# Kernel tuning notes

Measured on AMD Instinct MI355X. Metric: run time of the kernel, lower is better.

Reference implementation:

```python
import jax, jax.numpy as jnp
import numpy as np

N = 100_000        # num nodes
E = 1_600_000      # num edges (self-loops appended in reference)
IN_DIM = 128
OUT_DIM = 128
NUM_HEAD = 8
D_HEAD = OUT_DIM // NUM_HEAD
NEG_SLOPE = 0.2
EPS = 1e-10


def setup_inputs() -> dict:
    key = jax.random.key(0)
    k1, k2, k3, k4, k5 = jax.random.split(key, 5)
    x = jax.random.normal(k1, (N, IN_DIM), dtype=jnp.float32)
    edge_list = jax.random.randint(k2, (E, 2), 0, N, dtype=jnp.int32)
    edge_weight = jax.random.uniform(k3, (E,), dtype=jnp.float32)
    # nn.Linear(input_dim, output_dim) params
    W = jax.random.normal(k4, (IN_DIM, OUT_DIM), dtype=jnp.float32) / np.sqrt(IN_DIM).astype(np.float32)
    b = jnp.zeros((OUT_DIM,), dtype=jnp.float32)
    # query: (num_head, 2*output_dim/num_head), kaiming-uniform-ish init
    query = jax.random.normal(k5, (NUM_HEAD, 2 * D_HEAD), dtype=jnp.float32) * 0.1
    return {"x": x, "edge_list": edge_list, "edge_weight": edge_weight,
            "W": W, "b": b, "query": query}


def reference(x, edge_list, edge_weight, W, b, query):
    # --- message ---
    self_idx = jnp.arange(N, dtype=edge_list.dtype)
    node_in = jnp.concatenate([edge_list[:, 0], self_idx])   # [E+N]
    node_out = jnp.concatenate([edge_list[:, 1], self_idx])  # [E+N]
    ew = jnp.concatenate([edge_weight, jnp.ones((N,), edge_weight.dtype)])[:, None]  # [E+N,1]

    hidden = x @ W + b                                        # [N, OUT_DIM]
    h_in = hidden[node_in]                                    # [E+N, OUT_DIM]
    h_out = hidden[node_out]                                  # [E+N, OUT_DIM]

    # torch: stack(..., dim=-1).view(-1, num_head, 2*d_head) -> interleaved layout
    key_ = jnp.stack([h_in, h_out], axis=-1).reshape(-1, NUM_HEAD, 2 * D_HEAD)
    w = jnp.einsum('hd,nhd->nh', query, key_)                 # [E+N, H]
    w = jax.nn.leaky_relu(w, NEG_SLOPE)

    seg_max = jax.ops.segment_max(w, node_out, num_segments=N)  # [N, H]
    w = w - seg_max[node_out]
    att = jnp.exp(w) * ew                                     # [E+N, H]

    counts = jax.ops.segment_sum(jnp.ones((node_out.shape[0],), att.dtype),
                                 node_out, num_segments=N)[:, None]  # [N,1] (>=1: self-loops)
    norm = jax.ops.segment_sum(att, node_out, num_segments=N) / counts  # scatter_mean
    att = att / (norm[node_out] + EPS)

    value = h_in.reshape(-1, NUM_HEAD, D_HEAD)
    message = (att[..., None] * value).reshape(-1, OUT_DIM)   # [E+N, OUT_DIM]

    # --- aggregate: scatter_mean over node_out ---
    update = jax.ops.segment_sum(message, node_out, num_segments=N) / counts

    # --- combine: relu activation, no batch norm ---
    return jax.nn.relu(update)
```

## Files before the change

### kernel.cpp

```cpp
#include <hip/hip_runtime.h>

#define NH 8
#define DH 16
#define OD 128
#define NCH 256
#define NPB 128
#define ECAP 3072

typedef __attribute__((ext_vector_type(8))) short bf16x8;
typedef __attribute__((ext_vector_type(4))) float f32x4;

__device__ inline unsigned int f2bf(float f) {
    unsigned int u = __float_as_uint(f);
    return (u + 0x7fffu + ((u >> 16) & 1u)) >> 16;
}


__global__ __launch_bounds__(256) void binhist_kernel(const int2* __restrict__ el,
                                                      int* __restrict__ cnt,
                                                      int E, int total, int CH, int NB) {
    __shared__ int lh[1024];
    int t = threadIdx.x, c = blockIdx.x;
    for (int i = t; i < NB; i += 256) lh[i] = 0;
    __syncthreads();
    int beg = c * CH, end = min(total, beg + CH);
    for (int i = beg + t; i < end; i += 256) {
        int dst = (i < E) ? el[i].y : (i - E);
        atomicAdd(&lh[dst >> 7], 1);
    }
    __syncthreads();
    for (int i = t; i < NB; i += 256) cnt[i * NCH + c] = lh[i];
}

__global__ __launch_bounds__(1024) void scan1_kernel(const int* __restrict__ counts,
                                                     int* __restrict__ offsets,
                                                     int* __restrict__ bsums, int n) {
    __shared__ int tmp[1024];
    int t = threadIdx.x;
    int gid = blockIdx.x * 1024 + t;
    int v = (gid < n) ? counts[gid] : 0;
    tmp[t] = v;
    __syncthreads();
    int val = v;
    for (int off = 1; off < 1024; off <<= 1) {
        int add = (t >= off) ? tmp[t - off] : 0;
        __syncthreads();
        val += add;
        tmp[t] = val;
        __syncthreads();
    }
    if (gid < n) offsets[gid] = val - v;
    if (t == 1023) bsums[blockIdx.x] = val;
}

__global__ __launch_bounds__(1024) void scan2_kernel(int* __restrict__ bsums, int nb) {
    __shared__ int tmp[1024];
    int t = threadIdx.x;
    int v = (t < nb) ? bsums[t] : 0;
    tmp[t] = v;
    __syncthreads();
    int val = v;
    for (int off = 1; off < 1024; off <<= 1) {
        int add = (t >= off) ? tmp[t - off] : 0;
        __syncthreads();
        val += add;
        tmp[t] = val;
        __syncthreads();
    }
    if (t < nb) bsums[t] = val - v;
}

__global__ __launch_bounds__(1024) void scan3b_kernel(int* __restrict__ S,
                                                      const int* __restrict__ bsums,
                                                      const int* __restrict__ cnt, int n) {
    int gid = blockIdx.x * 1024 + threadIdx.x;
    if (gid < n) {
        int o = S[gid] + bsums[gid >> 10];
        S[gid] = o;
        if (gid == n - 1) S[n] = o + cnt[gid];
    }
}

__global__ __launch_bounds__(256) void binscatter_kernel(const int2* __restrict__ el,
                                                         const float* __restrict__ ew,
                                                         const int* __restrict__ S,
                                                         int2* __restrict__ binned,
                                                         int E, int total, int CH, int NB) {
    __shared__ int lcur[1024];
    int t = threadIdx.x, c = blockIdx.x;
    for (int i = t; i < NB; i += 256) lcur[i] = S[i * NCH + c];
    __syncthreads();
    int beg = c * CH, end = min(total, beg + CH);
    for (int i = beg + t; i < end; i += 256) {
        int src, dst; float w;
        if (i < E) { int2 e = el[i]; src = e.x; dst = e.y; w = ew[i]; }
        else       { src = dst = i - E; w = 1.0f; }
        int b = dst >> 7;
        int pos = atomicAdd(&lcur[b], 1);
        binned[pos] = make_int2(src | ((dst & 127) << 17), __float_as_int(w));
    }
}

__global__ __launch_bounds__(256) void binsort_kernel(const int2* __restrict__ binned,
                                                      const int* __restrict__ S,
                                                      int2* __restrict__ sedge,
                                                      int* __restrict__ offsets,
                                                      int N, int NB, int total) {
    __shared__ int2 eb[ECAP];
    __shared__ int lh[NPB];
    __shared__ int cu[NPB];
    int b = blockIdx.x, t = threadIdx.x;
    int base = S[b * NCH];
    int endb = S[(b + 1) * NCH];
    int cnt = min(endb - base, ECAP);

    for (int i = t; i < NPB; i += 256) lh[i] = 0;
    __syncthreads();
    for (int i = t; i < cnt; i += 256) {
        int2 e = binned[base + i];
        eb[i] = e;
        atomicAdd(&lh[(e.x >> 17) & 127], 1);
    }
    __syncthreads();
    if (t < 64) {
        int loc[2]; int s = 0;
#pragma unroll
        for (int j = 0; j < 2; ++j) { loc[j] = lh[t * 2 + j]; s += loc[j]; }
        int inc = s;
        for (int d = 1; d < 64; d <<= 1) {
            int o = __shfl_up(inc, d, 64);
            if (t >= d) inc += o;
        }
        int ex = inc - s;
#pragma unroll
        for (int j = 0; j < 2; ++j) { cu[t * 2 + j] = ex; ex += loc[j]; }
    }
    __syncthreads();
    int node0 = b << 7;
    for (int i = t; i < NPB; i += 256) {
        int node = node0 + i;
        if (node < N) offsets[node] = base + cu[i];
    }
    if (b == NB - 1 && t == 0) offsets[N] = total;
    __syncthreads();
    for (int i = t; i < cnt; i += 256) {
        int2 e = eb[i];
        int d = (e.x >> 17) & 127;
        int pos = atomicAdd(&cu[d], 1);
        sedge[base + pos] = e;
    }
}

__global__ __launch_bounds__(256) void gemm_proj_kernel(
        const float* __restrict__ x, const float* __restrict__ W,
        const float* __restrict__ b, const float* __restrict__ query,
        unsigned short* __restrict__ hbu, float* __restrict__ ain,
        float* __restrict__ aout, int N) {
    __shared__ unsigned short xs[64 * 136];
    __shared__ unsigned short wt[128 * 136];
    int t = threadIdx.x;
    int row0 = blockIdx.x * 64;

    {
        const float4* x4 = (const float4*)x;
#pragma unroll
        for (int i = 0; i < 8; ++i) {
            int f = t + i * 256;
            int row = f >> 5, c4 = f & 31;
            int gr = row0 + row;
            if (gr >= N) gr = N - 1;
            float4 v = x4[(size_t)gr * 32 + c4];
            unsigned int u0 = f2bf(v.x) | (f2bf(v.y) << 16);
            unsigned int u1 = f2bf(v.z) | (f2bf(v.w) << 16);
            *(uint2*)&xs[row * 136 + 4 * c4] = make_uint2(u0, u1);
        }
    }
    {
        const float4* W4 = (const float4*)W;
#pragma unroll
        for (int i = 0; i < 16; ++i) {
            int f = t + i * 256;
            int k = f & 127, c4 = f >> 7;
            float4 v = W4[k * 32 + c4];
            wt[(4 * c4 + 0) * 136 + k] = (unsigned short)f2bf(v.x);
            wt[(4 * c4 + 1) * 136 + k] = (unsigned short)f2bf(v.y);
            wt[(4 * c4 + 2) * 136 + k] = (unsigned short)f2bf(v.z);
            wt[(4 * c4 + 3) * 136 + k] = (unsigned short)f2bf(v.w);
        }
    }
    __syncthreads();

    int lane = t & 63, wv = t >> 6;
    int d = lane & 15, g = lane >> 4;
    int tbase = wv * 16;

    bf16x8 af[4];
#pragma unroll
    for (int s = 0; s < 4; ++s)
        af[s] = *(bf16x8*)&xs[(tbase + d) * 136 + s * 32 + g * 8];

    f32x4 acc[8];
#pragma unroll
    for (int c = 0; c < 8; ++c) acc[c] = (f32x4){0.f, 0.f, 0.f, 0.f};

#pragma unroll
    for (int c = 0; c < 8; ++c) {
#pragma unroll
        for (int s = 0; s < 4; ++s) {
            bf16x8 bf = *(bf16x8*)&wt[(d + 16 * c) * 136 + s * 32 + g * 8];
            acc[c] = __builtin_amdgcn_mfma_f32_16x16x32_bf16(af[s], bf, acc[c], 0, 0, 0);
        }
    }

    int rbase = row0 + tbase + g * 4;
#pragma unroll
    for (int c = 0; c < 8; ++c) {
        float bc = b[d + 16 * c];
        float2 q2 = *(const float2*)(query + c * 2 * DH + 2 * d);
#pragma unroll
        for (int j = 0; j < 4; ++j) {
            float v = acc[c][j] + bc;
            int row = rbase + j;
            if (row < N) hbu[(size_t)row * OD + d + 16 * c] = (unsigned short)f2bf(v);
            float pin = q2.x * v, pout = q2.y * v;
#pragma unroll
            for (int m = 1; m < 16; m <<= 1) {
                pin  += __shfl_xor(pin, m, 64);
                pout += __shfl_xor(pout, m, 64);
            }
            if (d == 0 && row < N) {
                ain[row * NH + c] = pin;
                aout[row * NH + c] = pout;
            }
        }
    }
}

__global__ __launch_bounds__(256) void edgeatt_kernel(
        const int* __restrict__ offsets, const int2* __restrict__ sedge,
        const float* __restrict__ ain, const float* __restrict__ aout,
        unsigned short* __restrict__ attB, int* __restrict__ srcArr,
        float* __restrict__ scaleG, int N) {
    int id = blockIdx.x * blockDim.x + threadIdx.x;
    int n = id >> 3, h = id & 7;
    if (n >= N) return;
    int beg = offsets[n], end = offsets[n + 1];
    float ao = aout[n * NH + h];

    float sum = 0.0f;
    int i = beg;
    for (; i + 1 < end; i += 2) {
        int2 e0 = sedge[i];
        int2 e1 = sedge[i + 1];
        int s0 = e0.x & 0x1FFFF, s1 = e1.x & 0x1FFFF;
        float a0 = ain[s0 * NH + h];
        float a1 = ain[s1 * NH + h];
        a0 += ao; a0 = (a0 > 0.0f) ? a0 : 0.2f * a0;
        a1 += ao; a1 = (a1 > 0.0f) ? a1 : 0.2f * a1;
        float t0 = __expf(a0) * __int_as_float(e0.y);
        float t1 = __expf(a1) * __int_as_float(e1.y);
        attB[(size_t)i * NH + h] = (unsigned short)f2bf(t0);
        attB[(size_t)(i + 1) * NH + h] = (unsigned short)f2bf(t1);
        sum += t0 + t1;
        if (h == 0) { srcArr[i] = s0; srcArr[i + 1] = s1; }
    }
    if (i < end) {
        int2 e0 = sedge[i];
        int s0 = e0.x & 0x1FFFF;
        float a0 = ain[s0 * NH + h] + ao;
        a0 = (a0 > 0.0f) ? a0 : 0.2f * a0;
        float t0 = __expf(a0) * __int_as_float(e0.y);
        attB[(size_t)i * NH + h] = (unsigned short)f2bf(t0);
        sum += t0;
        if (h == 0) srcArr[i] = s0;
    }
    float c = (float)(end - beg);
    scaleG[n * NH + h] = 1.0f / ((sum / c + 1e-10f) * c);
}

__global__ __launch_bounds__(256) void aggregate_kernel(
        const int* __restrict__ offsets, const int* __restrict__ srcArr,
        const unsigned short* __restrict__ attB, const float* __restrict__ scaleG,
        const uint2* __restrict__ hb2, float* __restrict__ out, int N) {
    int n = (blockIdx.x * blockDim.x + threadIdx.x) >> 6;
    int lane = threadIdx.x & 63;
    if (n >= N) return;
    int beg = offsets[n], end = offsets[n + 1];
    int half = lane >> 5, q = lane & 31;
    int h = q >> 2;

    float4 acc = make_float4(0.f, 0.f, 0.f, 0.f);
    for (int i = beg; i < end; i += 8) {
        int ib = i + 4 * half;
        int s[4]; float a[4];
#pragma unroll
        for (int k = 0; k < 4; ++k) {
            s[k] = srcArr[ib + k] & 0x1FFFF;
            a[k] = (ib + k < end)
                 ? __uint_as_float((unsigned int)attB[(size_t)(ib + k) * NH + h] << 16)
                 : 0.0f;
        }
        uint2 w[4];
#pragma unroll
        for (int k = 0; k < 4; ++k)
            w[k] = hb2[(size_t)s[k] * 32 + q];
#pragma unroll
        for (int k = 0; k < 4; ++k) {
            acc.x += a[k] * __uint_as_float(w[k].x << 16);
            acc.y += a[k] * __uint_as_float(w[k].x & 0xffff0000u);
            acc.z += a[k] * __uint_as_float(w[k].y << 16);
            acc.w += a[k] * __uint_as_float(w[k].y & 0xffff0000u);
        }
    }
    acc.x += __shfl_xor(acc.x, 32, 64);
    acc.y += __shfl_xor(acc.y, 32, 64);
    acc.z += __shfl_xor(acc.z, 32, 64);
    acc.w += __shfl_xor(acc.w, 32, 64);
    if (half == 0) {
        float sc = scaleG[n * NH + h];
        float4 o;
        o.x = acc.x * sc; o.y = acc.y * sc; o.z = acc.z * sc; o.w = acc.w * sc;
        o.x = o.x > 0.f ? o.x : 0.f;
        o.y = o.y > 0.f ? o.y : 0.f;
        o.z = o.z > 0.f ? o.z : 0.f;
        o.w = o.w > 0.f ? o.w : 0.f;
        *(float4*)(out + (size_t)n * OD + 4 * q) = o;
    }
}

extern "C" void kernel_launch(void* const* d_in, const int* in_sizes, int n_in,
                              void* d_out, int out_size, void* d_ws, size_t ws_size,
                              hipStream_t stream) {
    const float* x     = (const float*)d_in[0];
    const int2*  el    = (const int2*)d_in[1];
    const float* ew    = (const float*)d_in[2];
    const float* W     = (const float*)d_in[3];
    const float* b     = (const float*)d_in[4];
    const float* query = (const float*)d_in[5];
    float* out = (float*)d_out;

    int N = in_sizes[0] / OD;
    int E = in_sizes[1] / 2;
    int total = E + N;
    int NB = (N + NPB - 1) / NPB;
    int CH = (total + NCH - 1) / NCH;
    int n2 = NB * NCH;

    char* ws = (char*)d_ws;
    size_t off = 0;
    auto take = [&](size_t bytes) -> void* {
        void* p = ws + off;
        off = (off + bytes + 255) & ~(size_t)255;
        return p;
    };
    unsigned int* hb = (unsigned int*)take((size_t)N * 64 * 4);
    float* ain     = (float*)take((size_t)N * NH * 4);
    float* aout    = (float*)take((size_t)N * NH * 4);
    int*   cnt     = (int*)take((size_t)n2 * 4);
    int*   S       = (int*)take((size_t)(n2 + 1) * 4);
    int*   offsets = (int*)take((size_t)(N + 1) * 4);
    int*   bsums   = (int*)take(4096);
    int2*  binned  = (int2*)take((size_t)total * 8);
    int2*  sedge   = (int2*)take((size_t)total * 8);
    unsigned short* attB = (unsigned short*)take(((size_t)(total + 8) * NH) * 2);
    int*   srcArr  = (int*)binned;
    float* scaleG  = (float*)((char*)binned + ((size_t)total + 16) * 4);

    binhist_kernel<<<NCH, 256, 0, stream>>>(el, cnt, E, total, CH, NB);
    int nb = (n2 + 1023) / 1024;
    scan1_kernel<<<nb, 1024, 0, stream>>>(cnt, S, bsums, n2);
    scan2_kernel<<<1, 1024, 0, stream>>>(bsums, nb);
    scan3b_kernel<<<nb, 1024, 0, stream>>>(S, bsums, cnt, n2);
    binscatter_kernel<<<NCH, 256, 0, stream>>>(el, ew, S, binned, E, total, CH, NB);
    binsort_kernel<<<NB, 256, 0, stream>>>(binned, S, sedge, offsets, N, NB, total);
    gemm_proj_kernel<<<(N + 63) / 64, 256, 0, stream>>>(
        x, W, b, query, (unsigned short*)hb, ain, aout, N);
    edgeatt_kernel<<<((size_t)N * NH + 255) / 256, 256, 0, stream>>>(
        offsets, sedge, ain, aout, attB, srcArr, scaleG, N);
    aggregate_kernel<<<((size_t)N * 64 + 255) / 256, 256, 0, stream>>>(
        offsets, srcArr, attB, scaleG, (const uint2*)hb, out, N);
}
```

Baseline: 235.6 us.

## Store hidden and attention head-major and aggregate per head per block

The bf16 hidden features and edge attention weights move from node-major to head-major layout, and the aggregation kernel is reorganised so each block handles one head across four nodes. Each wavefront processes 16 edges at a time, with 4 lanes reading a 32-byte head slice, then reduces across lanes with shuffles. The intent is to make each head's gather footprint (1.6MB of hidden) small enough to stay in cache across the 8 head-blocks. The cost is that every edge's source index and offsets are now read 8 times, the gathers become 32-byte pieces instead of 256-byte rows, and the attention writes in edgeatt become strided.

```diff
diff --git a/kernel.cpp b/kernel.cpp
--- a/kernel.cpp
+++ b/kernel.cpp
@@ -221,7 +221,8 @@
         for (int j = 0; j < 4; ++j) {
             float v = acc[c][j] + bc;
             int row = rbase + j;
-            if (row < N) hbu[(size_t)row * OD + d + 16 * c] = (unsigned short)f2bf(v);
+            if (row < N)
+                hbu[(size_t)c * N * 16 + (size_t)row * 16 + d] = (unsigned short)f2bf(v);
             float pin = q2.x * v, pout = q2.y * v;
 #pragma unroll
             for (int m = 1; m < 16; m <<= 1) {
@@ -240,12 +241,13 @@
         const int* __restrict__ offsets, const int2* __restrict__ sedge,
         const float* __restrict__ ain, const float* __restrict__ aout,
         unsigned short* __restrict__ attB, int* __restrict__ srcArr,
-        float* __restrict__ scaleG, int N) {
+        float* __restrict__ scaleG, int N, int totalPad) {
     int id = blockIdx.x * blockDim.x + threadIdx.x;
     int n = id >> 3, h = id & 7;
     if (n >= N) return;
     int beg = offsets[n], end = offsets[n + 1];
     float ao = aout[n * NH + h];
+    unsigned short* attRow = attB + (size_t)h * totalPad;
 
     float sum = 0.0f;
     int i = beg;
@@ -259,8 +261,8 @@
         a1 += ao; a1 = (a1 > 0.0f) ? a1 : 0.2f * a1;
         float t0 = __expf(a0) * __int_as_float(e0.y);
         float t1 = __expf(a1) * __int_as_float(e1.y);
-        attB[(size_t)i * NH + h] = (unsigned short)f2bf(t0);
-        attB[(size_t)(i + 1) * NH + h] = (unsigned short)f2bf(t1);
+        attRow[i] = (unsigned short)f2bf(t0);
+        attRow[i + 1] = (unsigned short)f2bf(t1);
         sum += t0 + t1;
         if (h == 0) { srcArr[i] = s0; srcArr[i + 1] = s1; }
     }
@@ -270,7 +272,7 @@
         float a0 = ain[s0 * NH + h] + ao;
         a0 = (a0 > 0.0f) ? a0 : 0.2f * a0;
         float t0 = __expf(a0) * __int_as_float(e0.y);
-        attB[(size_t)i * NH + h] = (unsigned short)f2bf(t0);
+        attRow[i] = (unsigned short)f2bf(t0);
         sum += t0;
         if (h == 0) srcArr[i] = s0;
     }
@@ -281,50 +283,45 @@
 __global__ __launch_bounds__(256) void aggregate_kernel(
         const int* __restrict__ offsets, const int* __restrict__ srcArr,
         const unsigned short* __restrict__ attB, const float* __restrict__ scaleG,
-        const uint2* __restrict__ hb2, float* __restrict__ out, int N) {
-    int n = (blockIdx.x * blockDim.x + threadIdx.x) >> 6;
+        const uint2* __restrict__ hb2, float* __restrict__ out,
+        int N, int totalPad) {
+    int head = blockIdx.x & 7;
+    int n = (blockIdx.x >> 3) * 4 + (threadIdx.x >> 6);
     int lane = threadIdx.x & 63;
     if (n >= N) return;
     int beg = offsets[n], end = offsets[n + 1];
-    int half = lane >> 5, q = lane & 31;
-    int h = q >> 2;
+    int e = lane >> 2, q = lane & 3;
+    const unsigned short* attRow = attB + (size_t)head * totalPad;
+    const uint2* hbh = hb2 + (size_t)head * N * 4;
 
     float4 acc = make_float4(0.f, 0.f, 0.f, 0.f);
-    for (int i = beg; i < end; i += 8) {
-        int ib = i + 4 * half;
-        int s[4]; float a[4];
-#pragma unroll
-        for (int k = 0; k < 4; ++k) {
-            s[k] = srcArr[ib + k] & 0x1FFFF;
-            a[k] = (ib + k < end)
-                 ? __uint_as_float((unsigned int)attB[(size_t)(ib + k) * NH + h] << 16)
-                 : 0.0f;
-        }
-        uint2 w[4];
-#pragma unroll
-        for (int k = 0; k < 4; ++k)
-            w[k] = hb2[(size_t)s[k] * 32 + q];
-#pragma unroll
-        for (int k = 0; k < 4; ++k) {
-            acc.x += a[k] * __uint_as_float(w[k].x << 16);
-            acc.y += a[k] * __uint_as_float(w[k].x & 0xffff0000u);
-            acc.z += a[k] * __uint_as_float(w[k].y << 16);
-            acc.w += a[k] * __uint_as_float(w[k].y & 0xffff0000u);
-        }
-    }
-    acc.x += __shfl_xor(acc.x, 32, 64);
-    acc.y += __shfl_xor(acc.y, 32, 64);
-    acc.z += __shfl_xor(acc.z, 32, 64);
-    acc.w += __shfl_xor(acc.w, 32, 64);
-    if (half == 0) {
-        float sc = scaleG[n * NH + h];
+    for (int i = beg; i < end; i += 16) {
+        int idx = i + e;
+        int ic = (idx < end) ? idx : end - 1;
+        int s = srcArr[ic] & 0x1FFFF;
+        float a = (idx < end) ? __uint_as_float((unsigned int)attRow[ic] << 16) : 0.0f;
+        uint2 w = hbh[(size_t)s * 4 + q];
+        acc.x += a * __uint_as_float(w.x << 16);
+        acc.y += a * __uint_as_float(w.x & 0xffff0000u);
+        acc.z += a * __uint_as_float(w.y << 16);
+        acc.w += a * __uint_as_float(w.y & 0xffff0000u);
+    }
+#pragma unroll
+    for (int m = 4; m <= 32; m <<= 1) {
+        acc.x += __shfl_xor(acc.x, m, 64);
+        acc.y += __shfl_xor(acc.y, m, 64);
+        acc.z += __shfl_xor(acc.z, m, 64);
+        acc.w += __shfl_xor(acc.w, m, 64);
+    }
+    if (lane < 4) {
+        float sc = scaleG[n * NH + head];
         float4 o;
         o.x = acc.x * sc; o.y = acc.y * sc; o.z = acc.z * sc; o.w = acc.w * sc;
         o.x = o.x > 0.f ? o.x : 0.f;
         o.y = o.y > 0.f ? o.y : 0.f;
         o.z = o.z > 0.f ? o.z : 0.f;
         o.w = o.w > 0.f ? o.w : 0.f;
-        *(float4*)(out + (size_t)n * OD + 4 * q) = o;
+        *(float4*)(out + (size_t)n * OD + head * DH + 4 * q) = o;
     }
 }
 
@@ -342,6 +339,7 @@
     int N = in_sizes[0] / OD;
     int E = in_sizes[1] / 2;
     int total = E + N;
+    int totalPad = (total + 31) & ~31;
     int NB = (N + NPB - 1) / NPB;
     int CH = (total + NCH - 1) / NCH;
     int n2 = NB * NCH;
@@ -362,7 +360,7 @@
     int*   bsums   = (int*)take(4096);
     int2*  binned  = (int2*)take((size_t)total * 8);
     int2*  sedge   = (int2*)take((size_t)total * 8);
-    unsigned short* attB = (unsigned short*)take(((size_t)(total + 8) * NH) * 2);
+    unsigned short* attB = (unsigned short*)take((size_t)totalPad * NH * 2);
     int*   srcArr  = (int*)binned;
     float* scaleG  = (float*)((char*)binned + ((size_t)total + 16) * 4);
 
@@ -376,7 +374,7 @@
     gemm_proj_kernel<<<(N + 63) / 64, 256, 0, stream>>>(
         x, W, b, query, (unsigned short*)hb, ain, aout, N);
     edgeatt_kernel<<<((size_t)N * NH + 255) / 256, 256, 0, stream>>>(
-        offsets, sedge, ain, aout, attB, srcArr, scaleG, N);
-    aggregate_kernel<<<((size_t)N * 64 + 255) / 256, 256, 0, stream>>>(
-        offsets, srcArr, attB, scaleG, (const uint2*)hb, out, N);
-}
+        offsets, sedge, ain, aout, attB, srcArr, scaleG, N, totalPad);
+    aggregate_kernel<<<((N + 3) / 4) * 8, 256, 0, stream>>>(
+        offsets, srcArr, attB, scaleG, (const uint2*)hb, out, N, totalPad);
+}
```

Result: slower. 417.4 us (+77.2%).
